# Kernel optimization log

Measured on AMD Instinct MI355X. Metric: run time of the kernel, lower is better.

The kernel has to match this reference:

```python
import jax, jax.numpy as jnp
import numpy as np

B, W, F_IN = 128, 128, 64   # batch, window_size, num_features
N = 64                      # nodes per graph == num_features == tcn_out_channels
E = 4096                    # edges per graph
ED = 16                     # edge_feature_dim
H, C = 4, 32                # heads, gat_out_dim
FLAT = N * H * C            # 8192
HID = FLAT // 4             # 2048
LRELU_SLOPE = 0.01          # F.leaky_relu default
BN_EPS = 1e-5


def setup_inputs() -> dict:
    key = jax.random.key(0)
    ks = jax.random.split(key, 16)
    x = jax.random.normal(ks[0], (B, W, F_IN), jnp.float32)
    edge_index = jax.random.randint(ks[1], (2, E), 0, N)
    edge_attr = jax.random.normal(ks[2], (B, E, ED), jnp.float32)
    s = lambda k, shape, fan: jax.random.normal(k, shape, jnp.float32) / np.sqrt(fan)
    tcn_w = s(ks[3], (N, F_IN, 3), F_IN * 3)
    tcn_b = jnp.zeros((N,), jnp.float32)
    lin_l_w = s(ks[4], (H * C, W), W)
    lin_l_b = jnp.zeros((H * C,), jnp.float32)
    lin_e_w = s(ks[5], (H * C, ED), ED)
    lin_e_b = jnp.zeros((H * C,), jnp.float32)
    att = s(ks[6], (1, H, C), C)
    fc1_w = s(ks[7], (HID, FLAT), FLAT)
    fc1_b = jnp.zeros((HID,), jnp.float32)
    bn_g = jnp.ones((HID,), jnp.float32)
    bn_b = jnp.zeros((HID,), jnp.float32)
    fc2_w = s(ks[8], (2, HID), HID)
    fc2_b = jnp.zeros((2,), jnp.float32)
    return dict(x=x, edge_index=edge_index, edge_attr=edge_attr,
                tcn_w=tcn_w, tcn_b=tcn_b,
                lin_l_w=lin_l_w, lin_l_b=lin_l_b,
                lin_e_w=lin_e_w, lin_e_b=lin_e_b, att=att,
                fc1_w=fc1_w, fc1_b=fc1_b, bn_g=bn_g, bn_b=bn_b,
                fc2_w=fc2_w, fc2_b=fc2_b)


def reference(x, edge_index, edge_attr, tcn_w, tcn_b,
              lin_l_w, lin_l_b, lin_e_w, lin_e_b, att,
              fc1_w, fc1_b, bn_g, bn_b, fc2_w, fc2_b):
    # TCN: Conv1d(k=3, pad=1) over the window dim
    xt = jnp.transpose(x, (0, 2, 1))  # [B, F_IN, W]
    x_g = jax.lax.conv_general_dilated(
        xt, tcn_w, window_strides=(1,), padding=((1, 1),),
        dimension_numbers=('NCH', 'OIH', 'NCH')) + tcn_b[None, :, None]
    # x_g: [B, N, W] -> per-sample graph with N nodes, W-dim node features

    src, dst = edge_index[0], edge_index[1]

    def gat_one(xn, ea):
        # xn: [N, W], ea: [E, ED]
        h = (xn @ lin_l_w.T + lin_l_b).reshape(N, H, C)
        e = (ea @ lin_e_w.T + lin_e_b).reshape(E, H, C)
        xi = h[dst]               # [E, H, C] target node feats
        xj = h[src]               # [E, H, C] source node feats
        a = jax.nn.leaky_relu(xi + xj + e, LRELU_SLOPE)
        score = jnp.einsum('ehc,ohc->eh', a, att)  # [E, H]
        # segment softmax over edges grouped by destination node
        m = jax.ops.segment_max(score, dst, num_segments=N)
        m = jnp.where(jnp.isfinite(m), m, 0.0)
        ex = jnp.exp(score - m[dst])
        den = jax.ops.segment_sum(ex, dst, num_segments=N)
        alpha = ex / (den[dst] + 1e-16)            # [E, H]
        msg = xj * alpha[:, :, None]               # [E, H, C]
        out = jax.ops.segment_sum(msg, dst, num_segments=N)  # [N, H, C]
        return out.reshape(N, H * C)

    x_gat = jax.vmap(gat_one)(x_g, edge_attr)      # [B, N, H*C]
    x_gat = jax.nn.elu(x_gat)
    x_flat = x_gat.reshape(B, FLAT)

    h1 = x_flat @ fc1_w.T + fc1_b
    # BatchNorm1d in eval mode with fresh running stats (mean=0, var=1)
    h1 = h1 * (bn_g / jnp.sqrt(1.0 + BN_EPS)) + bn_b
    h1 = jax.nn.relu(h1)  # dropout is identity in eval
    logits = h1 @ fc2_w.T + fc2_b
    return logits
```

## Files before the change

kernel.cpp:

```cpp
#include <hip/hip_runtime.h>
#include <math.h>

#define BB   128
#define WW   128
#define FIN  64
#define NNODE 64
#define NE   4096
#define EDIM 16
#define NH   4
#define CDIM 32
#define HC   128
#define FLATD 8192
#define HIDD 2048

#define OFF_H    0u
#define OFF_P    1048576u
#define OFF_XGB  3211264u
#define OFF_BK   4259840u

typedef unsigned short u16;
typedef u16    u16x8  __attribute__((ext_vector_type(8)));
typedef u16    u16x4  __attribute__((ext_vector_type(4)));
typedef __bf16 bf16x8 __attribute__((ext_vector_type(8)));
typedef float  f32x4  __attribute__((ext_vector_type(4)));
typedef float  f32x16 __attribute__((ext_vector_type(16)));

__device__ __forceinline__ u16 f2bf(float f) {
    unsigned u = __float_as_uint(f);
    u += 0x7fffu + ((u >> 16) & 1u);
    return (u16)(u >> 16);
}
__device__ __forceinline__ void hilo(float v, u16* h, u16* l) {
    u16 hh = f2bf(v);
    float hf = __uint_as_float(((unsigned)hh) << 16);
    *h = hh;
    *l = f2bf(v - hf);
}

__global__ __launch_bounds__(256) void k0_bucket(
        const int* __restrict__ ei, int* __restrict__ bstart, int* __restrict__ blist)
{
    __shared__ int cnt[64];
    __shared__ int cur[65];
    const int t = threadIdx.x;
    if (t < 64) cnt[t] = 0;
    __syncthreads();
    for (int e = t; e < NE; e += 256) atomicAdd(&cnt[ei[NE + e]], 1);
    __syncthreads();
    if (t == 0) {
        int run = 0;
        for (int n = 0; n < 64; ++n) { cur[n] = run; run += cnt[n]; }
        cur[64] = run;
    }
    __syncthreads();
    if (t < 65) bstart[t] = cur[t];
    __syncthreads();
    for (int e = t; e < NE; e += 256) {
        int d = ei[NE + e], s = ei[e];
        int p = atomicAdd(&cur[d], 1);
        blist[p] = (e << 12) | (d << 6) | s;
    }
}

__global__ __launch_bounds__(256) void k1_tcn_linl(
        const float* __restrict__ x, const float* __restrict__ tcn_w,
        const float* __restrict__ tcn_b, const float* __restrict__ lin_l_w,
        const float* __restrict__ lin_l_b, float* __restrict__ h)
{
    __shared__ float xs[130*65];
    __shared__ float xg[32*132];
    const int b = blockIdx.x, half = blockIdx.y, t = threadIdx.x;
    const int n0 = half * 32;

    for (int idx = t; idx < 8192; idx += 256) {
        int w = idx >> 6, i = idx & 63;
        xs[(w+1)*65 + i] = x[b*8192 + idx];
    }
    if (t < 65) { xs[t] = 0.f; xs[129*65 + t] = 0.f; }
    __syncthreads();

    {
        const int nl = t >> 3;
        const int n  = n0 + nl;
        const int w0 = (t & 7) * 16;
        float acc[16];
        const float tb = tcn_b[n];
#pragma unroll
        for (int j = 0; j < 16; ++j) acc[j] = tb;
        for (int i = 0; i < 64; ++i) {
            const float t0 = tcn_w[n*192 + 3*i + 0];
            const float t1 = tcn_w[n*192 + 3*i + 1];
            const float t2 = tcn_w[n*192 + 3*i + 2];
            float a = xs[(w0+0)*65 + i];
            float c0 = xs[(w0+1)*65 + i];
#pragma unroll
            for (int dw = 0; dw < 16; ++dw) {
                float c = xs[(w0+dw+2)*65 + i];
                acc[dw] += a*t0 + c0*t1 + c*t2;
                a = c0; c0 = c;
            }
        }
#pragma unroll
        for (int dw = 0; dw < 16; ++dw) xg[nl*132 + w0 + dw] = acc[dw];
    }
    __syncthreads();

    {
        const int o2 = t & 63, ng = t >> 6;
        const int oA = o2, oB = o2 + 64;
        float accA[8], accB[8];
        const float lbA = lin_l_b[oA], lbB = lin_l_b[oB];
#pragma unroll
        for (int j = 0; j < 8; ++j) { accA[j] = lbA; accB[j] = lbB; }
        for (int c = 0; c < 32; ++c) {
            const float4 lwA = *(const float4*)&lin_l_w[oA*128 + c*4];
            const float4 lwB = *(const float4*)&lin_l_w[oB*128 + c*4];
#pragma unroll
            for (int nn = 0; nn < 8; ++nn) {
                const float4 xv = *(const float4*)&xg[(ng*8+nn)*132 + c*4];
                accA[nn] += xv.x*lwA.x + xv.y*lwA.y + xv.z*lwA.z + xv.w*lwA.w;
                accB[nn] += xv.x*lwB.x + xv.y*lwB.y + xv.z*lwB.z + xv.w*lwB.w;
            }
        }
#pragma unroll
        for (int nn = 0; nn < 8; ++nn) {
            const int n = n0 + ng*8 + nn;
            h[(b*64 + n)*128 + oA] = accA[nn];
            h[(b*64 + n)*128 + oB] = accB[nn];
        }
    }
}

#define CAPF 2560
__global__ __launch_bounds__(512, 1) void k2_fused(
        const float* __restrict__ hbase, const float* __restrict__ ea,
        const float* __restrict__ lin_e_w, const float* __restrict__ lin_e_b,
        const float* __restrict__ att, const int* __restrict__ bstart,
        const int* __restrict__ blist, u16* __restrict__ xgb)
{
    __shared__ float hbuf[64*132];
    __shared__ float scl[CAPF*4];
    __shared__ float Pm[4][32][68];
    __shared__ int   bst[33];
    const int b = blockIdx.x, half = blockIdx.y, t = threadIdx.x;
    const int lane = t & 63, wv = t >> 6, l32 = lane & 31, h5 = lane >> 5;

    for (int idx = t; idx < 8192; idx += 512) {
        const int o = idx & 127;
        hbuf[(idx>>7)*132 + o] = hbase[(size_t)b*8192 + idx] + 0.5f*lin_e_b[o];
    }
    for (int idx = t; idx < 4*32*68; idx += 512) ((float*)Pm)[idx] = 0.f;
    if (t < 33) bst[t] = bstart[half*32 + t];
    bf16x8 Ah[4], Al[4];
#pragma unroll
    for (int mt = 0; mt < 4; ++mt) {
        const float* wp = &lin_e_w[(mt*32 + l32)*16 + h5*8];
        const float4 w0 = *(const float4*)wp;
        const float4 w1 = *(const float4*)(wp + 4);
        u16 th[8], tl[8];
        hilo(w0.x,&th[0],&tl[0]); hilo(w0.y,&th[1],&tl[1]);
        hilo(w0.z,&th[2],&tl[2]); hilo(w0.w,&th[3],&tl[3]);
        hilo(w1.x,&th[4],&tl[4]); hilo(w1.y,&th[5],&tl[5]);
        hilo(w1.z,&th[6],&tl[6]); hilo(w1.w,&th[7],&tl[7]);
        u16x8 vh = { th[0],th[1],th[2],th[3],th[4],th[5],th[6],th[7] };
        u16x8 vl = { tl[0],tl[1],tl[2],tl[3],tl[4],tl[5],tl[6],tl[7] };
        Ah[mt] = *(bf16x8*)&vh;
        Al[mt] = *(bf16x8*)&vl;
    }
    float4 attv[4][4];
#pragma unroll
    for (int mt = 0; mt < 4; ++mt)
#pragma unroll
        for (int g = 0; g < 4; ++g)
            attv[mt][g] = *(const float4*)&att[mt*32 + g*8 + h5*4];
    __syncthreads();

    const int lo = bst[0], cnt = min(bst[32] - lo, CAPF);
    const int gcnt = (cnt + 31) >> 5;

    for (int g = wv; g < gcnt; g += 8) {
        const int idx = g*32 + l32;
        const bool valid = idx < cnt;
        const int pk = valid ? blist[lo + idx] : 0;
        const int sn = pk & 63, dd = (pk >> 6) & 63, e = pk >> 12;
        const float* eap = ea + ((size_t)b*NE + e)*16 + h5*8;
        const float4 v0 = *(const float4*)eap;
        const float4 v1 = *(const float4*)(eap + 4);
        u16 bh[8], bl[8];
        hilo(v0.x,&bh[0],&bl[0]); hilo(v0.y,&bh[1],&bl[1]);
        hilo(v0.z,&bh[2],&bl[2]); hilo(v0.w,&bh[3],&bl[3]);
        hilo(v1.x,&bh[4],&bl[4]); hilo(v1.y,&bh[5],&bl[5]);
        hilo(v1.z,&bh[6],&bl[6]); hilo(v1.w,&bh[7],&bl[7]);
        u16x8 vbh = { bh[0],bh[1],bh[2],bh[3],bh[4],bh[5],bh[6],bh[7] };
        u16x8 vbl = { bl[0],bl[1],bl[2],bl[3],bl[4],bl[5],bl[6],bl[7] };
        const bf16x8 Bh = *(bf16x8*)&vbh;
        const bf16x8 Bl = *(bf16x8*)&vbl;
        float hacc[4];
#pragma unroll
        for (int mt = 0; mt < 4; ++mt) {
            f32x16 D = {0.f,0.f,0.f,0.f,0.f,0.f,0.f,0.f,
                        0.f,0.f,0.f,0.f,0.f,0.f,0.f,0.f};
            D = __builtin_amdgcn_mfma_f32_32x32x16_bf16(Al[mt], Bh, D, 0, 0, 0);
            D = __builtin_amdgcn_mfma_f32_32x32x16_bf16(Ah[mt], Bl, D, 0, 0, 0);
            D = __builtin_amdgcn_mfma_f32_32x32x16_bf16(Ah[mt], Bh, D, 0, 0, 0);
            float s = 0.f;
#pragma unroll
            for (int g4 = 0; g4 < 4; ++g4) {
                const int ob = mt*32 + g4*8 + h5*4;
                const float4 hd = *(const float4*)&hbuf[dd*132 + ob];
                const float4 hs = *(const float4*)&hbuf[sn*132 + ob];
                float x0 = hd.x + hs.x + D[g4*4+0];
                float x1 = hd.y + hs.y + D[g4*4+1];
                float x2 = hd.z + hs.z + D[g4*4+2];
                float x3 = hd.w + hs.w + D[g4*4+3];
                x0 = fmaxf(x0, 0.01f*x0); x1 = fmaxf(x1, 0.01f*x1);
                x2 = fmaxf(x2, 0.01f*x2); x3 = fmaxf(x3, 0.01f*x3);
                const float4 a4 = attv[mt][g4];
                s += a4.x*x0 + a4.y*x1 + a4.z*x2 + a4.w*x3;
            }
            hacc[mt] = s;
        }
#pragma unroll
        for (int hh = 0; hh < 4; ++hh)
            hacc[hh] += __shfl_xor(hacc[hh], 32);
        if (h5 == 0 && valid)
            *(float4*)&scl[idx*4] = make_float4(hacc[0], hacc[1], hacc[2], hacc[3]);
    }
    __syncthreads();

    {
        const int pair = t >> 2, sub = t & 3;
        const int nl = pair >> 2, hh = pair & 3;
        const int s0 = bst[nl] - lo, s1 = bst[nl+1] - lo;
        float mx = -3.4e38f;
        for (int i = s0 + sub; i < s1; i += 4) mx = fmaxf(mx, scl[i*4 + hh]);
        mx = fmaxf(mx, __shfl_xor(mx, 1));
        mx = fmaxf(mx, __shfl_xor(mx, 2));
        float den = 0.f;
        for (int i = s0 + sub; i < s1; i += 4) {
            const float ex = __expf(scl[i*4 + hh] - mx);
            scl[i*4 + hh] = ex;
            den += ex;
        }
        den += __shfl_xor(den, 1);
        den += __shfl_xor(den, 2);
        const float rd = 1.0f / (den + 1e-16f);
        for (int i = s0 + sub; i < s1; i += 4) {
            const int src = blist[lo + i] & 63;
            atomicAdd(&Pm[hh][nl][src], scl[i*4 + hh] * rd);
        }
    }
    __syncthreads();

    if (wv < 4) {
        const int hh = wv;
        f32x16 D = {0.f,0.f,0.f,0.f,0.f,0.f,0.f,0.f,
                    0.f,0.f,0.f,0.f,0.f,0.f,0.f,0.f};
#pragma unroll
        for (int k0 = 0; k0 < 64; k0 += 16) {
            const float* pp = &Pm[hh][l32][k0 + h5*8];
            const float4 a0 = *(const float4*)pp;
            const float4 a1 = *(const float4*)(pp + 4);
            u16 ph[8], pl[8];
            hilo(a0.x,&ph[0],&pl[0]); hilo(a0.y,&ph[1],&pl[1]);
            hilo(a0.z,&ph[2],&pl[2]); hilo(a0.w,&ph[3],&pl[3]);
            hilo(a1.x,&ph[4],&pl[4]); hilo(a1.y,&ph[5],&pl[5]);
            hilo(a1.z,&ph[6],&pl[6]); hilo(a1.w,&ph[7],&pl[7]);
            u16x8 vph = { ph[0],ph[1],ph[2],ph[3],ph[4],ph[5],ph[6],ph[7] };
            u16x8 vpl = { pl[0],pl[1],pl[2],pl[3],pl[4],pl[5],pl[6],pl[7] };
            u16 hhv[8], hlv[8];
#pragma unroll
            for (int i = 0; i < 8; ++i) {
                const float v = hbuf[(k0 + h5*8 + i)*132 + hh*32 + l32];
                hilo(v, &hhv[i], &hlv[i]);
            }
            u16x8 vhh = { hhv[0],hhv[1],hhv[2],hhv[3],hhv[4],hhv[5],hhv[6],hhv[7] };
            u16x8 vhl = { hlv[0],hlv[1],hlv[2],hlv[3],hlv[4],hlv[5],hlv[6],hlv[7] };
            const bf16x8 Ph = *(bf16x8*)&vph, Pl = *(bf16x8*)&vpl;
            const bf16x8 Hh = *(bf16x8*)&vhh, Hl = *(bf16x8*)&vhl;
            D = __builtin_amdgcn_mfma_f32_32x32x16_bf16(Pl, Hh, D, 0, 0, 0);
            D = __builtin_amdgcn_mfma_f32_32x32x16_bf16(Ph, Hl, D, 0, 0, 0);
            D = __builtin_amdgcn_mfma_f32_32x32x16_bf16(Ph, Hh, D, 0, 0, 0);
        }
        const int c = l32, o = hh*32 + c;
        const float lb2 = 0.5f * lin_e_b[o];
#pragma unroll
        for (int r = 0; r < 16; ++r) {
            const int m = (r & 3) + 8*(r >> 2) + 4*h5;
            const float corr = (bst[m+1] > bst[m]) ? lb2 : 0.f;
            float v = D[r] - corr;
            v = v > 0.f ? v : expm1f(v);
            xgb[(size_t)b*8192 + (half*32 + m)*128 + o] = f2bf(v);
        }
    }
}

__global__ __launch_bounds__(256) void k3_fc1(
        const u16* __restrict__ xgb, const float* __restrict__ fc1_w,
        float* __restrict__ part)
{
    __shared__ u16 Ash[128*72];
    __shared__ u16 Bsh[32*72];
    const int jb = blockIdx.x, ks = blockIdx.y, t = threadIdx.x;
    const int j0 = jb*32, k0 = ks*1024;
    const int wave = t >> 6, lane = t & 63;
    const int quad = lane >> 4, l16 = lane & 15;
    const int wm = (wave & 1) * 64, wn = (wave >> 1) * 16;

    f32x4 acc[4];
#pragma unroll
    for (int i = 0; i < 4; ++i) acc[i] = (f32x4){0.f, 0.f, 0.f, 0.f};

    const int arow = t >> 1, acol = (t & 1) * 32;
    const int brow = t >> 3, bcol = (t & 7) * 8;

    for (int kc = 0; kc < 1024; kc += 64) {
        if (kc) __syncthreads();
        const u16* ap = xgb + (size_t)arow*FLATD + k0 + kc + acol;
#pragma unroll
        for (int qq = 0; qq < 4; ++qq)
            *(u16x8*)&Ash[arow*72 + acol + qq*8] = *(const u16x8*)(ap + qq*8);
        const float* bp = fc1_w + (size_t)(j0 + brow)*FLATD + k0 + kc + bcol;
        {
            float4 v0 = *(const float4*)(bp);
            float4 v1 = *(const float4*)(bp + 4);
            u16x8 u = { f2bf(v0.x), f2bf(v0.y), f2bf(v0.z), f2bf(v0.w),
                        f2bf(v1.x), f2bf(v1.y), f2bf(v1.z), f2bf(v1.w) };
            *(u16x8*)&Bsh[brow*72 + bcol] = u;
        }
        __syncthreads();
#pragma unroll
        for (int kk = 0; kk < 64; kk += 32) {
            bf16x8 af[4], bfr;
#pragma unroll
            for (int i = 0; i < 4; ++i)
                af[i] = *(const bf16x8*)&Ash[(wm + i*16 + l16)*72 + kk + quad*8];
            bfr = *(const bf16x8*)&Bsh[(wn + l16)*72 + kk + quad*8];
#pragma unroll
            for (int i = 0; i < 4; ++i)
                acc[i] = __builtin_amdgcn_mfma_f32_16x16x32_bf16(af[i], bfr, acc[i], 0, 0, 0);
        }
    }
#pragma unroll
    for (int i = 0; i < 4; ++i) {
        const int n = j0 + wn + l16;
#pragma unroll
        for (int r = 0; r < 4; ++r) {
            const int m = wm + i*16 + quad*4 + r;
            part[(size_t)ks*262144 + (size_t)m*HIDD + n] = acc[i][r];
        }
    }
}

__global__ __launch_bounds__(256) void k4_fc2(
        const float* __restrict__ part, const float* __restrict__ fc1_b,
        const float* __restrict__ bn_g, const float* __restrict__ bn_b,
        const float* __restrict__ fc2_w, const float* __restrict__ fc2_b,
        float* __restrict__ out)
{
    __shared__ float r0[256], r1[256];
    const int b = blockIdx.x, t = threadIdx.x;
    const float inv = 1.0f / sqrtf(1.0f + 1e-5f);
    float p0 = 0.f, p1 = 0.f;
    for (int j = t; j < 2048; j += 256) {
        float hv = 0.f;
#pragma unroll
        for (int s = 0; s < 8; ++s) hv += part[(size_t)s*262144 + (size_t)b*2048 + j];
        float v = (hv + fc1_b[j]) * (bn_g[j] * inv) + bn_b[j];
        v = fmaxf(v, 0.f);
        p0 += v * fc2_w[j];
        p1 += v * fc2_w[2048 + j];
    }
    r0[t] = p0; r1[t] = p1;
    __syncthreads();
    for (int s = 128; s > 0; s >>= 1) {
        if (t < s) { r0[t] += r0[t+s]; r1[t] += r1[t+s]; }
        __syncthreads();
    }
    if (t == 0) {
        out[b*2 + 0] = r0[0] + fc2_b[0];
        out[b*2 + 1] = r1[0] + fc2_b[1];
    }
}

extern "C" void kernel_launch(void* const* d_in, const int* in_sizes, int n_in,
                              void* d_out, int out_size, void* d_ws, size_t ws_size,
                              hipStream_t stream)
{
    const float* x       = (const float*)d_in[0];
    const int*   ei      = (const int*)  d_in[1];
    const float* ea      = (const float*)d_in[2];
    const float* tcn_w   = (const float*)d_in[3];
    const float* tcn_b   = (const float*)d_in[4];
    const float* lin_l_w = (const float*)d_in[5];
    const float* lin_l_b = (const float*)d_in[6];
    const float* lin_e_w = (const float*)d_in[7];
    const float* lin_e_b = (const float*)d_in[8];
    const float* att     = (const float*)d_in[9];
    const float* fc1_w   = (const float*)d_in[10];
    const float* fc1_b   = (const float*)d_in[11];
    const float* bn_g    = (const float*)d_in[12];
    const float* bn_b    = (const float*)d_in[13];
    const float* fc2_w   = (const float*)d_in[14];
    const float* fc2_b   = (const float*)d_in[15];

    float* ws     = (float*)d_ws;
    float* hbuf   = ws + OFF_H;
    float* part   = ws + OFF_P;
    u16*   xgb    = (u16*)(ws + OFF_XGB);
    int*   bstart = (int*)(ws + OFF_BK);
    int*   blist  = bstart + 80;
    float* out    = (float*)d_out;

    k0_bucket  <<<1, 256, 0, stream>>>(ei, bstart, blist);
    k1_tcn_linl<<<dim3(BB, 2), 256, 0, stream>>>(x, tcn_w, tcn_b, lin_l_w, lin_l_b, hbuf);
    k2_fused   <<<dim3(BB, 2), 512, 0, stream>>>(hbuf, ea, lin_e_w, lin_e_b, att,
                                                 bstart, blist, xgb);
    k3_fc1     <<<dim3(64, 8), 256, 0, stream>>>(xgb, fc1_w, part);
    k4_fc2     <<<BB, 256, 0, stream>>>(part, fc1_b, bn_g, bn_b, fc2_w, fc2_b, out);
}
```

Before: 248.0 us.

## Split GAT fused kernel into quarter-node blocks with 16x16 MFMA aggregation

The fused GAT kernel now runs four blocks per sample, each owning 16 destination nodes instead of 32. This doubles the grid and shrinks each block's shared-memory footprint, which should allow more blocks per CU. The aggregation GEMM switches from 32x32x16 to 16x16x32 MFMA so all eight waves take part. The softmax reduction uses eight lanes per node-head pair, and the h staging and Pm zeroing use float4 stores. In exchange, each sample's h tile is loaded from global memory twice as often. The per-block edge capacity also drops to 1600, which relies on per-quarter edge counts staying under that bound.

```diff
diff --git a/kernel.cpp b/kernel.cpp
--- a/kernel.cpp
+++ b/kernel.cpp
@@ -131,8 +131,8 @@
     }
 }
 
-#define CAPF 2560
-__global__ __launch_bounds__(512, 1) void k2_fused(
+#define CAPF 1600
+__global__ __launch_bounds__(512, 4) void k2_fused(
         const float* __restrict__ hbase, const float* __restrict__ ea,
         const float* __restrict__ lin_e_w, const float* __restrict__ lin_e_b,
         const float* __restrict__ att, const int* __restrict__ bstart,
@@ -140,17 +140,24 @@
 {
     __shared__ float hbuf[64*132];
     __shared__ float scl[CAPF*4];
-    __shared__ float Pm[4][32][68];
-    __shared__ int   bst[33];
-    const int b = blockIdx.x, half = blockIdx.y, t = threadIdx.x;
+    __shared__ float Pm[4][16][68];
+    __shared__ int   bst[17];
+    const int b = blockIdx.x, quart = blockIdx.y, t = threadIdx.x;
     const int lane = t & 63, wv = t >> 6, l32 = lane & 31, h5 = lane >> 5;
 
-    for (int idx = t; idx < 8192; idx += 512) {
-        const int o = idx & 127;
-        hbuf[(idx>>7)*132 + o] = hbase[(size_t)b*8192 + idx] + 0.5f*lin_e_b[o];
-    }
-    for (int idx = t; idx < 4*32*68; idx += 512) ((float*)Pm)[idx] = 0.f;
-    if (t < 33) bst[t] = bstart[half*32 + t];
+    for (int idx = t; idx < 2048; idx += 512) {
+        const int row = idx >> 5, c4 = (idx & 31) * 4;
+        float4 hv = *(const float4*)&hbase[(size_t)b*8192 + row*128 + c4];
+        const float4 eb = *(const float4*)&lin_e_b[c4];
+        hv.x += 0.5f*eb.x; hv.y += 0.5f*eb.y;
+        hv.z += 0.5f*eb.z; hv.w += 0.5f*eb.w;
+        *(float4*)&hbuf[row*132 + c4] = hv;
+    }
+    {
+        const f32x4 z4 = {0.f, 0.f, 0.f, 0.f};
+        for (int idx = t; idx < 4*16*68/4; idx += 512) ((f32x4*)Pm)[idx] = z4;
+    }
+    if (t < 17) bst[t] = bstart[quart*16 + t];
     bf16x8 Ah[4], Al[4];
 #pragma unroll
     for (int mt = 0; mt < 4; ++mt) {
@@ -175,7 +182,7 @@
             attv[mt][g] = *(const float4*)&att[mt*32 + g*8 + h5*4];
     __syncthreads();
 
-    const int lo = bst[0], cnt = min(bst[32] - lo, CAPF);
+    const int lo = bst[0], cnt = min(bst[16] - lo, CAPF);
     const int gcnt = (cnt + 31) >> 5;
 
     for (int g = wv; g < gcnt; g += 8) {
@@ -229,36 +236,39 @@
     __syncthreads();
 
     {
-        const int pair = t >> 2, sub = t & 3;
+        const int pair = t >> 3, sub = t & 7;
         const int nl = pair >> 2, hh = pair & 3;
         const int s0 = bst[nl] - lo, s1 = bst[nl+1] - lo;
         float mx = -3.4e38f;
-        for (int i = s0 + sub; i < s1; i += 4) mx = fmaxf(mx, scl[i*4 + hh]);
+        for (int i = s0 + sub; i < s1; i += 8) mx = fmaxf(mx, scl[i*4 + hh]);
         mx = fmaxf(mx, __shfl_xor(mx, 1));
         mx = fmaxf(mx, __shfl_xor(mx, 2));
+        mx = fmaxf(mx, __shfl_xor(mx, 4));
         float den = 0.f;
-        for (int i = s0 + sub; i < s1; i += 4) {
+        for (int i = s0 + sub; i < s1; i += 8) {
             const float ex = __expf(scl[i*4 + hh] - mx);
             scl[i*4 + hh] = ex;
             den += ex;
         }
         den += __shfl_xor(den, 1);
         den += __shfl_xor(den, 2);
+        den += __shfl_xor(den, 4);
         const float rd = 1.0f / (den + 1e-16f);
-        for (int i = s0 + sub; i < s1; i += 4) {
+        for (int i = s0 + sub; i < s1; i += 8) {
             const int src = blist[lo + i] & 63;
             atomicAdd(&Pm[hh][nl][src], scl[i*4 + hh] * rd);
         }
     }
     __syncthreads();
 
-    if (wv < 4) {
-        const int hh = wv;
-        f32x16 D = {0.f,0.f,0.f,0.f,0.f,0.f,0.f,0.f,
-                    0.f,0.f,0.f,0.f,0.f,0.f,0.f,0.f};
-#pragma unroll
-        for (int k0 = 0; k0 < 64; k0 += 16) {
-            const float* pp = &Pm[hh][l32][k0 + h5*8];
+    {
+        const int hh = wv >> 1, ct = wv & 1;
+        const int l16 = lane & 15, q = lane >> 4;
+        const int cb = hh*32 + ct*16 + l16;
+        f32x4 D = {0.f, 0.f, 0.f, 0.f};
+#pragma unroll
+        for (int k0 = 0; k0 < 64; k0 += 32) {
+            const float* pp = &Pm[hh][l16][k0 + q*8];
             const float4 a0 = *(const float4*)pp;
             const float4 a1 = *(const float4*)(pp + 4);
             u16 ph[8], pl[8];
@@ -271,26 +281,25 @@
             u16 hhv[8], hlv[8];
 #pragma unroll
             for (int i = 0; i < 8; ++i) {
-                const float v = hbuf[(k0 + h5*8 + i)*132 + hh*32 + l32];
+                const float v = hbuf[(k0 + q*8 + i)*132 + cb];
                 hilo(v, &hhv[i], &hlv[i]);
             }
             u16x8 vhh = { hhv[0],hhv[1],hhv[2],hhv[3],hhv[4],hhv[5],hhv[6],hhv[7] };
             u16x8 vhl = { hlv[0],hlv[1],hlv[2],hlv[3],hlv[4],hlv[5],hlv[6],hlv[7] };
             const bf16x8 Ph = *(bf16x8*)&vph, Pl = *(bf16x8*)&vpl;
             const bf16x8 Hh = *(bf16x8*)&vhh, Hl = *(bf16x8*)&vhl;
-            D = __builtin_amdgcn_mfma_f32_32x32x16_bf16(Pl, Hh, D, 0, 0, 0);
-            D = __builtin_amdgcn_mfma_f32_32x32x16_bf16(Ph, Hl, D, 0, 0, 0);
-            D = __builtin_amdgcn_mfma_f32_32x32x16_bf16(Ph, Hh, D, 0, 0, 0);
-        }
-        const int c = l32, o = hh*32 + c;
-        const float lb2 = 0.5f * lin_e_b[o];
-#pragma unroll
-        for (int r = 0; r < 16; ++r) {
-            const int m = (r & 3) + 8*(r >> 2) + 4*h5;
+            D = __builtin_amdgcn_mfma_f32_16x16x32_bf16(Pl, Hh, D, 0, 0, 0);
+            D = __builtin_amdgcn_mfma_f32_16x16x32_bf16(Ph, Hl, D, 0, 0, 0);
+            D = __builtin_amdgcn_mfma_f32_16x16x32_bf16(Ph, Hh, D, 0, 0, 0);
+        }
+        const float lb2 = 0.5f * lin_e_b[cb];
+#pragma unroll
+        for (int r = 0; r < 4; ++r) {
+            const int m = q*4 + r;
             const float corr = (bst[m+1] > bst[m]) ? lb2 : 0.f;
             float v = D[r] - corr;
             v = v > 0.f ? v : expm1f(v);
-            xgb[(size_t)b*8192 + (half*32 + m)*128 + o] = f2bf(v);
+            xgb[(size_t)b*8192 + (quart*16 + m)*128 + cb] = f2bf(v);
         }
     }
 }
@@ -414,7 +423,7 @@
 
     k0_bucket  <<<1, 256, 0, stream>>>(ei, bstart, blist);
     k1_tcn_linl<<<dim3(BB, 2), 256, 0, stream>>>(x, tcn_w, tcn_b, lin_l_w, lin_l_b, hbuf);
-    k2_fused   <<<dim3(BB, 2), 512, 0, stream>>>(hbuf, ea, lin_e_w, lin_e_b, att,
+    k2_fused   <<<dim3(BB, 4), 512, 0, stream>>>(hbuf, ea, lin_e_w, lin_e_b, att,
                                                  bstart, blist, xgb);
     k3_fc1     <<<dim3(64, 8), 256, 0, stream>>>(xgb, fc1_w, part);
     k4_fc2     <<<BB, 256, 0, stream>>>(part, fc1_b, bn_g, bn_b, fc2_w, fc2_b, out);
```

Measured after the change: 297.8 us. 1.2x slower.
